# Kernel tuning notes

Hardware: AMD Instinct MI355X
Metric: run time of the kernel (lower is better)

Reference implementation:

```python
import jax, jax.numpy as jnp
import numpy as np

B, S, H, I, E = 4, 4096, 1024, 4096, 4
VOCAB = 32000


def setup_inputs() -> dict:
    key = jax.random.key(0)
    k1, k2, k3, k4, k5 = jax.random.split(key, 5)
    scale = 1.0 / np.sqrt(H)
    return {
        "hidden_states": jax.random.normal(k1, (B, S, H), dtype=jnp.float32),
        "gate_proj": jax.random.normal(k2, (E, H, I), dtype=jnp.float32) * scale,
        "up_proj": jax.random.normal(k3, (E, H, I), dtype=jnp.float32) * scale,
        "down_proj": jax.random.normal(k4, (E, I, H), dtype=jnp.float32) * (1.0 / np.sqrt(I)),
        "token_ids": jax.random.randint(k5, (B, S), 0, VOCAB, dtype=jnp.int64),
    }


def reference(hidden_states, gate_proj, up_proj, down_proj, token_ids):
    # hidden_states: [B, S, H]; token_ids: [B, S]
    num_experts = gate_proj.shape[0]
    expert_ids = token_ids % num_experts  # [B, S]
    out = jnp.zeros_like(hidden_states)
    for e in range(num_experts):  # small fixed expert loop
        gate = jax.nn.silu(jnp.einsum("bsh,hi->bsi", hidden_states, gate_proj[e]))
        up = jnp.einsum("bsh,hi->bsi", hidden_states, up_proj[e])
        y = jnp.einsum("bsi,ih->bsh", gate * up, down_proj[e])
        out = jnp.where((expert_ids == e)[..., None], y, out)
    return out
```

## Files before the change

kernel.cpp:

```cpp
#include <hip/hip_runtime.h>

#define TOK    16384
#define HD     1024
#define ID     4096
#define NE     4
#define MAXMT  131
#define MAXMT2 67
#define NKT    (HD / 64)

typedef __attribute__((ext_vector_type(4))) float f32x4;
typedef __attribute__((ext_vector_type(8))) short bf16x8;
typedef unsigned int u32;

static __device__ __forceinline__ unsigned short f2bf(float f) {
  unsigned u = __float_as_uint(f);
  u += 0x7FFFu + ((u >> 16) & 1u);
  return (unsigned short)(u >> 16);
}

static __device__ __forceinline__ void gl16(const void* g, void* l) {
  __builtin_amdgcn_global_load_lds((const __attribute__((address_space(1))) u32*)g,
                                   (__attribute__((address_space(3))) u32*)l, 16, 0, 0);
}

static __device__ __forceinline__ void barx() {
  asm volatile("" ::: "memory");
  __builtin_amdgcn_s_barrier();
  asm volatile("" ::: "memory");
}

__global__ void k_route0(const int* __restrict__ ids, int* __restrict__ meta) {
  __shared__ int cnt[4];
  int t = threadIdx.x;
  if (t < 4) cnt[t] = 0;
  __syncthreads();
  int l0 = 0, l1 = 0, l2 = 0, l3 = 0;
  for (int i = t; i < TOK; i += 256) {
    int e = ids[i] & 3;
    l0 += (e == 0); l1 += (e == 1); l2 += (e == 2); l3 += (e == 3);
  }
  atomicAdd(&cnt[0], l0); atomicAdd(&cnt[1], l1);
  atomicAdd(&cnt[2], l2); atomicAdd(&cnt[3], l3);
  __syncthreads();
  if (t == 0) {
    int o = 0;
    for (int e = 0; e < 4; ++e) { meta[e] = o; meta[8 + e] = o; o += cnt[e]; }
    meta[4] = o;
  }
}

__global__ void k_route1(const int* __restrict__ ids, int* __restrict__ meta,
                         int* __restrict__ perm) {
  int i = blockIdx.x * 256 + threadIdx.x;
  if (i < TOK) {
    int e = ids[i] & 3;
    int s = atomicAdd(&meta[8 + e], 1);
    perm[s] = i;
  }
}

__global__ void k_conv(const float* __restrict__ s, unsigned short* __restrict__ d, int n8) {
  int i = blockIdx.x * blockDim.x + threadIdx.x;
  int st = gridDim.x * blockDim.x;
  for (; i < n8; i += st) {
    const f32x4* p = (const f32x4*)(s + ((size_t)i << 3));
    f32x4 a = p[0], b = p[1];
    union { unsigned short u[8]; uint4 q; } o;
    o.u[0] = f2bf(a.x); o.u[1] = f2bf(a.y); o.u[2] = f2bf(a.z); o.u[3] = f2bf(a.w);
    o.u[4] = f2bf(b.x); o.u[5] = f2bf(b.y); o.u[6] = f2bf(b.z); o.u[7] = f2bf(b.w);
    *(uint4*)(d + ((size_t)i << 3)) = o.q;
  }
}

__global__ void k_tr12(const float* __restrict__ gw, const float* __restrict__ uw,
                       const float* __restrict__ dw, unsigned short* __restrict__ gT,
                       unsigned short* __restrict__ uT, unsigned short* __restrict__ dT) {
  __shared__ float tile[64][65];
  int z = blockIdx.y;
  const float* s; unsigned short* d; int R, C, lg;
  if (z < 8) {
    R = HD; C = ID; lg = 6;
    int m = z & 3;
    if (z < 4) { s = gw + (size_t)m * R * C; d = gT + (size_t)m * R * C; }
    else       { s = uw + (size_t)m * R * C; d = uT + (size_t)m * R * C; }
  } else {
    R = ID; C = HD; lg = 4;
    int m = z - 8;
    s = dw + (size_t)m * R * C; d = dT + (size_t)m * R * C;
  }
  int bx = blockIdx.x;
  int tx = bx & ((1 << lg) - 1), ty = bx >> lg;
  int r0 = ty << 6, c0 = tx << 6;
  int t = threadIdx.x;
  int lr = t >> 4, lc = (t & 15) << 2;
  #pragma unroll
  for (int it = 0; it < 4; ++it) {
    int r = lr + (it << 4);
    f32x4 v = *(const f32x4*)(s + (size_t)(r0 + r) * C + c0 + lc);
    tile[r][lc] = v.x; tile[r][lc + 1] = v.y; tile[r][lc + 2] = v.z; tile[r][lc + 3] = v.w;
  }
  __syncthreads();
  int c = t >> 2, rb = (t & 3) << 4;
  union { unsigned short u[16]; uint4 q[2]; } o;
  #pragma unroll
  for (int j = 0; j < 16; ++j) o.u[j] = f2bf(tile[rb + j][c]);
  uint4* dp = (uint4*)(d + (size_t)(c0 + c) * R + r0 + rb);
  dp[0] = o.q[0]; dp[1] = o.q[1];
}

#define MFMA16 __builtin_amdgcn_mfma_f32_16x16x32_bf16

#define RD_A(MH, KX, D) { _Pragma("unroll") for (int m = 0; m < 4; ++m) \
  fa[m] = *(const bf16x8*)(smem + (D) + ((offA[m] + (MH) * 8192) ^ ((KX) << 6))); }
#define RD_B(KX, D) { _Pragma("unroll") for (int n = 0; n < 4; ++n) \
  fb[n] = *(const bf16x8*)(smem + (D) + (offB[n] ^ ((KX) << 6))); }
#define STG_A(HH, TILE, D) { _Pragma("unroll") for (int j = (HH) * 2; j < (HH) * 2 + 2; ++j) \
  gl16(srcA[j] + (TILE) * 64, smem + (D) + dstA[j]); }
#define STG_B(HH, TILE, D) { _Pragma("unroll") for (int j = (HH) * 2; j < (HH) * 2 + 2; ++j) \
  gl16(srcB[j] + (TILE) * 64, smem + (D) + dstB[j]); }
#define PH_TAIL(MH) barx(); \
  asm volatile("s_waitcnt lgkmcnt(0)" ::: "memory"); \
  __builtin_amdgcn_sched_barrier(0); \
  __builtin_amdgcn_s_setprio(1); \
  { _Pragma("unroll") for (int m = 0; m < 4; ++m) \
    _Pragma("unroll") for (int n = 0; n < 4; ++n) \
      acc[(MH) * 4 + m][n] = MFMA16(fa[m], fb[n], acc[(MH) * 4 + m][n], 0, 0, 0); } \
  __builtin_amdgcn_s_setprio(0)

__global__ __launch_bounds__(512, 2) void k_gemm1(
    const unsigned short* __restrict__ hid,
    const unsigned short* __restrict__ gT,
    const unsigned short* __restrict__ uT,
    const int* __restrict__ meta,
    const int* __restrict__ perm,
    unsigned short* __restrict__ act) {
  extern __shared__ __align__(16) char smem[];
  int offs[5];
  #pragma unroll
  for (int i = 0; i < 5; ++i) offs[i] = meta[i];
  int bid = blockIdx.x;
  int logical = (bid & 7) * (MAXMT2 * 32 / 8) + (bid >> 3);
  int mt = logical >> 5;
  int ny = logical & 31;
  int e = -1, mloc = 0, base = 0;
  #pragma unroll
  for (int ee = 0; ee < 4; ++ee) {
    int tiles = (offs[ee + 1] - offs[ee] + 255) >> 8;
    if (e < 0 && mt < base + tiles) { e = ee; mloc = mt - base; }
    base += tiles;
  }
  if (e < 0) return;
  int slot0 = offs[e] + (mloc << 8);
  int send = offs[e + 1];
  int tid = threadIdx.x, lane = tid & 63, wid = tid >> 6;
  int n0 = ny << 7;

  int rsub = lane >> 3;
  int ke = ((lane & 7) ^ rsub) << 3;
  const unsigned short* srcA[4];
  const unsigned short* srcB[4];
  int dstA[4], dstB[4];
  const unsigned short* gb = gT + (size_t)e * ID * HD;
  const unsigned short* ub = uT + (size_t)e * ID * HD;
  #pragma unroll
  for (int j = 0; j < 4; ++j) {
    int r = j * 64 + wid * 8 + rsub;
    int slot = slot0 + r;
    int pr = perm[slot < send ? slot : slot0];
    srcA[j] = hid + (size_t)pr * HD + ke;
    dstA[j] = j * 8192 + wid * 1024;
    int rb = r;
    int s = rb >> 4;
    int grow = n0 + ((s >> 1) << 4) + (rb & 15);
    srcB[j] = ((s & 1) ? ub : gb) + (size_t)grow * HD + ke;
    dstB[j] = 32768 + j * 8192 + wid * 1024;
  }

  int wm = wid >> 2, wn = wid & 3;
  int r16 = lane & 15, kg = lane >> 4;
  int offA[4], offB[4];
  #pragma unroll
  for (int m = 0; m < 4; ++m) {
    int row = wm * 128 + m * 16 + r16;
    offA[m] = row * 128 + ((kg << 4) ^ ((row & 7) << 4));
  }
  #pragma unroll
  for (int n = 0; n < 4; ++n) {
    int row = wn * 64 + n * 16 + r16;
    offB[n] = 32768 + row * 128 + ((kg << 4) ^ ((row & 7) << 4));
  }

  f32x4 acc[8][4];
  #pragma unroll
  for (int m = 0; m < 8; ++m)
    #pragma unroll
    for (int n = 0; n < 4; ++n) acc[m][n] = (f32x4){0.f, 0.f, 0.f, 0.f};
  bf16x8 fa[4], fb[4];

  STG_B(0, 0, 0);
  STG_A(0, 0, 0); STG_A(1, 0, 0);
  STG_B(1, 0, 0);
  STG_B(0, 1, 65536);
  asm volatile("s_waitcnt vmcnt(2)" ::: "memory");
  barx();

  #pragma unroll 1
  for (int i = 0; i < NKT / 2 - 1; ++i) {
    int t1 = 2 * i + 1, t2 = 2 * i + 2, t3 = 2 * i + 3;
    RD_A(0, 0, 0); RD_B(0, 0);
    STG_B(1, t1, 65536);
    PH_TAIL(0); barx();
    RD_A(1, 0, 0);
    STG_A(0, t1, 65536); STG_A(1, t1, 65536);
    PH_TAIL(1); barx();
    RD_A(0, 1, 0); RD_B(1, 0);
    PH_TAIL(0); barx();
    RD_A(1, 1, 0);
    STG_B(0, t2, 0);
    PH_TAIL(1);
    asm volatile("s_waitcnt vmcnt(2)" ::: "memory");
    barx();
    RD_A(0, 0, 65536); RD_B(0, 65536);
    STG_A(0, t2, 0); STG_A(1, t2, 0);
    PH_TAIL(0); barx();
    RD_A(1, 0, 65536);
    STG_B(1, t2, 0);
    PH_TAIL(1); barx();
    RD_A(0, 1, 65536); RD_B(1, 65536);
    PH_TAIL(0); barx();
    RD_A(1, 1, 65536);
    STG_B(0, t3, 65536);
    PH_TAIL(1);
    asm volatile("s_waitcnt vmcnt(2)" ::: "memory");
    barx();
  }
  {
    RD_A(0, 0, 0); RD_B(0, 0);
    STG_B(1, 15, 65536);
    PH_TAIL(0); barx();
    RD_A(1, 0, 0);
    STG_A(0, 15, 65536); STG_A(1, 15, 65536);
    PH_TAIL(1); barx();
    RD_A(0, 1, 0); RD_B(1, 0);
    PH_TAIL(0); barx();
    RD_A(1, 1, 0);
    PH_TAIL(1);
    asm volatile("s_waitcnt vmcnt(0)" ::: "memory");
    barx();
    RD_A(0, 0, 65536); RD_B(0, 65536);
    PH_TAIL(0); barx();
    RD_A(1, 0, 65536);
    PH_TAIL(1); barx();
    RD_A(0, 1, 65536); RD_B(1, 65536);
    PH_TAIL(0); barx();
    RD_A(1, 1, 65536);
    PH_TAIL(1);
  }

  #pragma unroll
  for (int mf = 0; mf < 8; ++mf) {
    int lr = wm * 128 + mf * 16 + kg * 4;
    #pragma unroll
    for (int np = 0; np < 2; ++np) {
      int col = n0 + (2 * wn + np) * 16 + r16;
      #pragma unroll
      for (int r = 0; r < 4; ++r) {
        int slot = slot0 + lr + r;
        if (slot < send) {
          float g = acc[mf][2 * np][r];
          float u = acc[mf][2 * np + 1][r];
          float y = (g / (1.f + __expf(-g))) * u;
          act[(size_t)slot * ID + col] = f2bf(y);
        }
      }
    }
  }
}

__global__ __launch_bounds__(256, 2) void k_gemm2(
    const unsigned short* __restrict__ act,
    const unsigned short* __restrict__ dT,
    const int* __restrict__ meta,
    const int* __restrict__ perm,
    float* __restrict__ out) {
  __shared__ unsigned short As[128 * 64];
  __shared__ unsigned short Bs[128 * 64];
  int offs[5];
  #pragma unroll
  for (int i = 0; i < 5; ++i) offs[i] = meta[i];
  int bid = blockIdx.x;
  int logical = (bid & 7) * (MAXMT * 8 / 8) + (bid >> 3);
  int mt = logical >> 3;
  int nyy = logical & 7;
  int e = -1, mloc = 0, base = 0;
  #pragma unroll
  for (int ee = 0; ee < 4; ++ee) {
    int tiles = (offs[ee + 1] - offs[ee] + 127) >> 7;
    if (e < 0 && mt < base + tiles) { e = ee; mloc = mt - base; }
    base += tiles;
  }
  if (e < 0) return;
  int slot0 = offs[e] + (mloc << 7);
  int send = offs[e + 1];
  int tid = threadIdx.x;
  int n0 = nyy << 7;
  const unsigned short* dbase = dT + (size_t)e * HD * ID;
  const unsigned short* ap[4];
  const unsigned short* bp[4];
  int wofs[4];
  #pragma unroll
  for (int it = 0; it < 4; ++it) {
    int b = (tid << 4) + (it << 12);
    int row = b >> 7;
    int kob = b & 127;
    int slot = slot0 + row;
    int s2 = slot < send ? slot : slot0;
    ap[it] = act + (size_t)s2 * ID + (kob >> 1);
    bp[it] = dbase + (size_t)(n0 + row) * ID + (kob >> 1);
    wofs[it] = row * 64 + ((kob ^ ((row & 7) << 4)) >> 1);
  }
  int lane = tid & 63, wid = tid >> 6;
  int wm = wid >> 1, wn = wid & 1;
  int r16 = lane & 15, kg = lane >> 4;
  f32x4 zero = {0.f, 0.f, 0.f, 0.f};
  f32x4 acc[4][4];
  #pragma unroll
  for (int m = 0; m < 4; ++m)
    #pragma unroll
    for (int n = 0; n < 4; ++n) acc[m][n] = zero;

  bf16x8 sa[4], sb[4];
  #pragma unroll
  for (int it = 0; it < 4; ++it) {
    sa[it] = *(const bf16x8*)(ap[it]);
    sb[it] = *(const bf16x8*)(bp[it]);
  }
  for (int kt = 0; kt < ID / 64; ++kt) {
    __syncthreads();
    #pragma unroll
    for (int it = 0; it < 4; ++it) {
      *(bf16x8*)(As + wofs[it]) = sa[it];
      *(bf16x8*)(Bs + wofs[it]) = sb[it];
    }
    __syncthreads();
    if (kt < ID / 64 - 1) {
      int ko = (kt + 1) << 6;
      #pragma unroll
      for (int it = 0; it < 4; ++it) {
        sa[it] = *(const bf16x8*)(ap[it] + ko);
        sb[it] = *(const bf16x8*)(bp[it] + ko);
      }
    }
    #pragma unroll
    for (int kk = 0; kk < 2; ++kk) {
      bf16x8 fa[4], fb[4];
      #pragma unroll
      for (int m = 0; m < 4; ++m) {
        int row = (wm << 6) + (m << 4) + r16;
        int kob = (kk << 6) + (kg << 4);
        fa[m] = *(const bf16x8*)(As + row * 64 + ((kob ^ ((row & 7) << 4)) >> 1));
      }
      #pragma unroll
      for (int n = 0; n < 4; ++n) {
        int row = (wn << 6) + (n << 4) + r16;
        int kob = (kk << 6) + (kg << 4);
        fb[n] = *(const bf16x8*)(Bs + row * 64 + ((kob ^ ((row & 7) << 4)) >> 1));
      }
      #pragma unroll
      for (int m = 0; m < 4; ++m)
        #pragma unroll
        for (int n = 0; n < 4; ++n)
          acc[m][n] = __builtin_amdgcn_mfma_f32_16x16x32_bf16(fa[m], fb[n], acc[m][n], 0, 0, 0);
    }
  }
  #pragma unroll
  for (int m = 0; m < 4; ++m) {
    int lr = (wm << 6) + (m << 4) + (kg << 2);
    int pr4[4];
    #pragma unroll
    for (int r = 0; r < 4; ++r) {
      int slot = slot0 + lr + r;
      pr4[r] = slot < send ? perm[slot] : -1;
    }
    #pragma unroll
    for (int n = 0; n < 4; ++n) {
      int col = n0 + (wn << 6) + (n << 4) + r16;
      #pragma unroll
      for (int r = 0; r < 4; ++r) {
        if (pr4[r] >= 0) out[(size_t)pr4[r] * HD + col] = acc[m][n][r];
      }
    }
  }
}

extern "C" void kernel_launch(void* const* d_in, const int* in_sizes, int n_in,
                              void* d_out, int out_size, void* d_ws, size_t ws_size,
                              hipStream_t stream) {
  const float* hs = (const float*)d_in[0];
  const float* gw = (const float*)d_in[1];
  const float* uw = (const float*)d_in[2];
  const float* dw = (const float*)d_in[3];
  const int* ids = (const int*)d_in[4];
  float* out = (float*)d_out;

  char* w = (char*)d_ws;
  size_t o = 0;
  int* meta = (int*)(w + o); o += 64;
  int* perm = (int*)(w + o); o += (size_t)TOK * 4;
  o = (o + 255) & ~(size_t)255;
  unsigned short* hid = (unsigned short*)(w + o); o += (size_t)TOK * HD * 2;
  unsigned short* gT  = (unsigned short*)(w + o); o += (size_t)NE * ID * HD * 2;
  unsigned short* uT  = (unsigned short*)(w + o); o += (size_t)NE * ID * HD * 2;
  unsigned short* dT  = (unsigned short*)(w + o); o += (size_t)NE * ID * HD * 2;
  unsigned short* actb = (unsigned short*)(w + o); o += (size_t)TOK * ID * 2;

  hipFuncSetAttribute((const void*)k_gemm1,
                      hipFuncAttributeMaxDynamicSharedMemorySize, 131072);

  hipLaunchKernelGGL(k_route0, dim3(1), dim3(256), 0, stream, ids, meta);
  hipLaunchKernelGGL(k_route1, dim3(TOK / 256), dim3(256), 0, stream, ids, meta, perm);
  hipLaunchKernelGGL(k_conv, dim3(2048), dim3(256), 0, stream, hs, hid, TOK * HD / 8);
  hipLaunchKernelGGL(k_tr12, dim3(1024, 12), dim3(256), 0, stream, gw, uw, dw, gT, uT, dT);
  hipLaunchKernelGGL(k_gemm1, dim3(MAXMT2 * 32), dim3(512), 131072, stream,
                     hid, gT, uT, meta, perm, actb);
  hipLaunchKernelGGL(k_gemm2, dim3(MAXMT * 8), dim3(256), 0, stream,
                     actb, dT, meta, perm, out);
}
```

Baseline: 666.9 us.

## Restructure gemm1 pipeline to 4-stage K=32 ring buffer with double-buffered fragments

Replaces the two-stage K=64 LDS double buffer in the gate/up GEMM with a four-deep ring of K=32 tiles (32 KB each) and a new XOR swizzle sized for 64-byte rows. Register fragments are double-buffered (faX/faY, fbE/fbO), so LDS reads for the next MFMA cluster are issued before the current one and waited on with partial lgkmcnt counts. The aim is deeper global-load prefetch and better overlap of LDS reads with MFMA. In exchange it uses more fragment registers, issues more barriers per unit of K, and the clamped tail stages issue redundant loads.

```diff
diff --git a/kernel.cpp b/kernel.cpp
--- a/kernel.cpp
+++ b/kernel.cpp
@@ -6,7 +6,7 @@
 #define NE     4
 #define MAXMT  131
 #define MAXMT2 67
-#define NKT    (HD / 64)
+#define NT32   (HD / 32)
 
 typedef __attribute__((ext_vector_type(4))) float f32x4;
 typedef __attribute__((ext_vector_type(8))) short bf16x8;
@@ -109,22 +109,27 @@
 }
 
 #define MFMA16 __builtin_amdgcn_mfma_f32_16x16x32_bf16
-
-#define RD_A(MH, KX, D) { _Pragma("unroll") for (int m = 0; m < 4; ++m) \
-  fa[m] = *(const bf16x8*)(smem + (D) + ((offA[m] + (MH) * 8192) ^ ((KX) << 6))); }
-#define RD_B(KX, D) { _Pragma("unroll") for (int n = 0; n < 4; ++n) \
-  fb[n] = *(const bf16x8*)(smem + (D) + (offB[n] ^ ((KX) << 6))); }
-#define STG_A(HH, TILE, D) { _Pragma("unroll") for (int j = (HH) * 2; j < (HH) * 2 + 2; ++j) \
-  gl16(srcA[j] + (TILE) * 64, smem + (D) + dstA[j]); }
-#define STG_B(HH, TILE, D) { _Pragma("unroll") for (int j = (HH) * 2; j < (HH) * 2 + 2; ++j) \
-  gl16(srcB[j] + (TILE) * 64, smem + (D) + dstB[j]); }
-#define PH_TAIL(MH) barx(); \
-  asm volatile("s_waitcnt lgkmcnt(0)" ::: "memory"); \
+#define BASE4(T) (((T) & 3) * 32768)
+
+#define RD1(T, FA, FB) { const char* bb = smem + BASE4(T); \
+  _Pragma("unroll") for (int m = 0; m < 4; ++m) FA[m] = *(const bf16x8*)(bb + offA0[m]); \
+  _Pragma("unroll") for (int n = 0; n < 4; ++n) FB[n] = *(const bf16x8*)(bb + offB[n]); }
+
+#define RD2(T, FA) { const char* bb = smem + BASE4(T); \
+  _Pragma("unroll") for (int m = 0; m < 4; ++m) FA[m] = *(const bf16x8*)(bb + offA1[m]); }
+
+#define STG(T, H) { int tt = (T) < NT32 ? (T) : NT32 - 1; int ko = tt * 32; \
+  char* bb = smem + BASE4(T); \
+  gl16(srcA[H] + ko, bb + dA[H]); gl16(srcB[H] + ko, bb + dB[H]); }
+
+#define CLUSTER(FA, FB, MH, NW) \
+  barx(); \
+  asm volatile("s_waitcnt lgkmcnt(" #NW ")" ::: "memory"); \
   __builtin_amdgcn_sched_barrier(0); \
   __builtin_amdgcn_s_setprio(1); \
   { _Pragma("unroll") for (int m = 0; m < 4; ++m) \
     _Pragma("unroll") for (int n = 0; n < 4; ++n) \
-      acc[(MH) * 4 + m][n] = MFMA16(fa[m], fb[n], acc[(MH) * 4 + m][n], 0, 0, 0); } \
+      acc[(MH) * 4 + m][n] = MFMA16(FA[m], FB[n], acc[(MH) * 4 + m][n], 0, 0, 0); } \
   __builtin_amdgcn_s_setprio(0)
 
 __global__ __launch_bounds__(512, 2) void k_gemm1(
@@ -155,39 +160,40 @@
   int tid = threadIdx.x, lane = tid & 63, wid = tid >> 6;
   int n0 = ny << 7;
 
-  int rsub = lane >> 3;
-  int ke = ((lane & 7) ^ rsub) << 3;
-  const unsigned short* srcA[4];
-  const unsigned short* srcB[4];
-  int dstA[4], dstB[4];
+  int sslot = (tid & 3) ^ ((tid >> 3) & 3);
+  int ke = sslot << 3;
+  const unsigned short* srcA[2];
+  const unsigned short* srcB[2];
+  int dA[2], dB[2];
   const unsigned short* gb = gT + (size_t)e * ID * HD;
   const unsigned short* ub = uT + (size_t)e * ID * HD;
   #pragma unroll
-  for (int j = 0; j < 4; ++j) {
-    int r = j * 64 + wid * 8 + rsub;
+  for (int j = 0; j < 2; ++j) {
+    int r = (tid >> 2) + j * 128;
     int slot = slot0 + r;
     int pr = perm[slot < send ? slot : slot0];
     srcA[j] = hid + (size_t)pr * HD + ke;
-    dstA[j] = j * 8192 + wid * 1024;
-    int rb = r;
-    int s = rb >> 4;
-    int grow = n0 + ((s >> 1) << 4) + (rb & 15);
-    srcB[j] = ((s & 1) ? ub : gb) + (size_t)grow * HD + ke;
-    dstB[j] = 32768 + j * 8192 + wid * 1024;
+    dA[j] = (tid << 4) + j * 8192;
+    int sB = r >> 4;
+    int grow = n0 + ((sB >> 1) << 4) + (r & 15);
+    srcB[j] = ((sB & 1) ? ub : gb) + (size_t)grow * HD + ke;
+    dB[j] = 16384 + (tid << 4) + j * 8192;
   }
 
   int wm = wid >> 2, wn = wid & 3;
   int r16 = lane & 15, kg = lane >> 4;
-  int offA[4], offB[4];
+  int offA0[4], offA1[4], offB[4];
   #pragma unroll
   for (int m = 0; m < 4; ++m) {
-    int row = wm * 128 + m * 16 + r16;
-    offA[m] = row * 128 + ((kg << 4) ^ ((row & 7) << 4));
+    int r0 = wm * 128 + m * 16 + r16;
+    offA0[m] = r0 * 64 + ((kg << 4) ^ (((r0 >> 1) & 3) << 4));
+    int r1 = r0 + 64;
+    offA1[m] = r1 * 64 + ((kg << 4) ^ (((r1 >> 1) & 3) << 4));
   }
   #pragma unroll
   for (int n = 0; n < 4; ++n) {
-    int row = wn * 64 + n * 16 + r16;
-    offB[n] = 32768 + row * 128 + ((kg << 4) ^ ((row & 7) << 4));
+    int rb = wn * 64 + n * 16 + r16;
+    offB[n] = 16384 + rb * 64 + ((kg << 4) ^ (((rb >> 1) & 3) << 4));
   }
 
   f32x4 acc[8][4];
@@ -195,67 +201,34 @@
   for (int m = 0; m < 8; ++m)
     #pragma unroll
     for (int n = 0; n < 4; ++n) acc[m][n] = (f32x4){0.f, 0.f, 0.f, 0.f};
-  bf16x8 fa[4], fb[4];
-
-  STG_B(0, 0, 0);
-  STG_A(0, 0, 0); STG_A(1, 0, 0);
-  STG_B(1, 0, 0);
-  STG_B(0, 1, 65536);
-  asm volatile("s_waitcnt vmcnt(2)" ::: "memory");
+  bf16x8 faX[4], faY[4], fbE[4], fbO[4];
+
+  STG(0, 0); STG(0, 1);
+  STG(1, 0); STG(1, 1);
+  STG(2, 0);
+  asm volatile("s_waitcnt vmcnt(6)" ::: "memory");
   barx();
+  RD1(0, faX, fbE);
 
   #pragma unroll 1
-  for (int i = 0; i < NKT / 2 - 1; ++i) {
-    int t1 = 2 * i + 1, t2 = 2 * i + 2, t3 = 2 * i + 3;
-    RD_A(0, 0, 0); RD_B(0, 0);
-    STG_B(1, t1, 65536);
-    PH_TAIL(0); barx();
-    RD_A(1, 0, 0);
-    STG_A(0, t1, 65536); STG_A(1, t1, 65536);
-    PH_TAIL(1); barx();
-    RD_A(0, 1, 0); RD_B(1, 0);
-    PH_TAIL(0); barx();
-    RD_A(1, 1, 0);
-    STG_B(0, t2, 0);
-    PH_TAIL(1);
-    asm volatile("s_waitcnt vmcnt(2)" ::: "memory");
-    barx();
-    RD_A(0, 0, 65536); RD_B(0, 65536);
-    STG_A(0, t2, 0); STG_A(1, t2, 0);
-    PH_TAIL(0); barx();
-    RD_A(1, 0, 65536);
-    STG_B(1, t2, 0);
-    PH_TAIL(1); barx();
-    RD_A(0, 1, 65536); RD_B(1, 65536);
-    PH_TAIL(0); barx();
-    RD_A(1, 1, 65536);
-    STG_B(0, t3, 65536);
-    PH_TAIL(1);
-    asm volatile("s_waitcnt vmcnt(2)" ::: "memory");
-    barx();
-  }
-  {
-    RD_A(0, 0, 0); RD_B(0, 0);
-    STG_B(1, 15, 65536);
-    PH_TAIL(0); barx();
-    RD_A(1, 0, 0);
-    STG_A(0, 15, 65536); STG_A(1, 15, 65536);
-    PH_TAIL(1); barx();
-    RD_A(0, 1, 0); RD_B(1, 0);
-    PH_TAIL(0); barx();
-    RD_A(1, 1, 0);
-    PH_TAIL(1);
-    asm volatile("s_waitcnt vmcnt(0)" ::: "memory");
-    barx();
-    RD_A(0, 0, 65536); RD_B(0, 65536);
-    PH_TAIL(0); barx();
-    RD_A(1, 0, 65536);
-    PH_TAIL(1); barx();
-    RD_A(0, 1, 65536); RD_B(1, 65536);
-    PH_TAIL(0); barx();
-    RD_A(1, 1, 65536);
-    PH_TAIL(1);
-  }
+  for (int i = 0; i < NT32 / 2; ++i) {
+    int te = 2 * i, to = 2 * i + 1;
+    RD2(te, faY);
+    STG(te + 2, 1);
+    asm volatile("s_waitcnt vmcnt(4)" ::: "memory");
+    CLUSTER(faX, fbE, 0, 4);
+    RD1(to, faX, fbO);
+    STG(te + 3, 0);
+    CLUSTER(faY, fbE, 1, 8);
+    RD2(to, faY);
+    STG(te + 3, 1);
+    asm volatile("s_waitcnt vmcnt(4)" ::: "memory");
+    CLUSTER(faX, fbO, 0, 4);
+    RD1(te + 2, faX, fbE);
+    STG(te + 4, 0);
+    CLUSTER(faY, fbO, 1, 8);
+  }
+  asm volatile("s_waitcnt vmcnt(0) lgkmcnt(0)" ::: "memory");
 
   #pragma unroll
   for (int mf = 0; mf < 8; ++mf) {
```

New measurement: 694.0 us. 1.04x slower.

## Widen down-proj GEMM tile to 128x256 with 8 waves; fuse prep kernels

Applied to the files above, without the earlier changes.

The hidden-state bf16 conversion and the weight transpose kernels are merged into a single launch with a 2D grid, which removes one launch and lets the two overlap. The second GEMM now uses 512 threads, a 128x256 output tile and a larger B shared buffer. The grid drops to 524 blocks with a new XCD-aware mapping in which M tiles vary fastest, aiming for more reuse of A per loaded tile and better L2 locality. The cost is more LDS per block and fewer blocks in flight, which may reduce occupancy.

```diff
diff --git a/kernel.cpp b/kernel.cpp
--- a/kernel.cpp
+++ b/kernel.cpp
@@ -59,24 +59,23 @@
   }
 }
 
-__global__ void k_conv(const float* __restrict__ s, unsigned short* __restrict__ d, int n8) {
-  int i = blockIdx.x * blockDim.x + threadIdx.x;
-  int st = gridDim.x * blockDim.x;
-  for (; i < n8; i += st) {
-    const f32x4* p = (const f32x4*)(s + ((size_t)i << 3));
+__global__ void k_pre(const float* __restrict__ gw, const float* __restrict__ uw,
+                      const float* __restrict__ dw, const float* __restrict__ hs,
+                      unsigned short* __restrict__ gT, unsigned short* __restrict__ uT,
+                      unsigned short* __restrict__ dT, unsigned short* __restrict__ hid) {
+  int z = blockIdx.y;
+  int t = threadIdx.x;
+  if (z >= 12) {
+    int i = ((z - 12) * 1024 + blockIdx.x) * 256 + t;
+    const f32x4* p = (const f32x4*)(hs + ((size_t)i << 3));
     f32x4 a = p[0], b = p[1];
     union { unsigned short u[8]; uint4 q; } o;
     o.u[0] = f2bf(a.x); o.u[1] = f2bf(a.y); o.u[2] = f2bf(a.z); o.u[3] = f2bf(a.w);
     o.u[4] = f2bf(b.x); o.u[5] = f2bf(b.y); o.u[6] = f2bf(b.z); o.u[7] = f2bf(b.w);
-    *(uint4*)(d + ((size_t)i << 3)) = o.q;
-  }
-}
-
-__global__ void k_tr12(const float* __restrict__ gw, const float* __restrict__ uw,
-                       const float* __restrict__ dw, unsigned short* __restrict__ gT,
-                       unsigned short* __restrict__ uT, unsigned short* __restrict__ dT) {
+    *(uint4*)(hid + ((size_t)i << 3)) = o.q;
+    return;
+  }
   __shared__ float tile[64][65];
-  int z = blockIdx.y;
   const float* s; unsigned short* d; int R, C, lg;
   if (z < 8) {
     R = HD; C = ID; lg = 6;
@@ -91,7 +90,6 @@
   int bx = blockIdx.x;
   int tx = bx & ((1 << lg) - 1), ty = bx >> lg;
   int r0 = ty << 6, c0 = tx << 6;
-  int t = threadIdx.x;
   int lr = t >> 4, lc = (t & 15) << 2;
   #pragma unroll
   for (int it = 0; it < 4; ++it) {
@@ -277,21 +275,23 @@
   }
 }
 
-__global__ __launch_bounds__(256, 2) void k_gemm2(
+__global__ __launch_bounds__(512, 2) void k_gemm2(
     const unsigned short* __restrict__ act,
     const unsigned short* __restrict__ dT,
     const int* __restrict__ meta,
     const int* __restrict__ perm,
     float* __restrict__ out) {
   __shared__ unsigned short As[128 * 64];
-  __shared__ unsigned short Bs[128 * 64];
+  __shared__ unsigned short Bs[256 * 64];
   int offs[5];
   #pragma unroll
   for (int i = 0; i < 5; ++i) offs[i] = meta[i];
   int bid = blockIdx.x;
-  int logical = (bid & 7) * (MAXMT * 8 / 8) + (bid >> 3);
-  int mt = logical >> 3;
-  int nyy = logical & 7;
+  int xcd = bid & 7, off = bid >> 3;
+  int q = 524 / 8, r = 524 % 8;
+  int logical = (xcd < r ? xcd * (q + 1) : r * (q + 1) + (xcd - r) * q) + off;
+  int mt = logical % MAXMT;
+  int nyy = logical / MAXMT;
   int e = -1, mloc = 0, base = 0;
   #pragma unroll
   for (int ee = 0; ee < 4; ++ee) {
@@ -303,53 +303,56 @@
   int slot0 = offs[e] + (mloc << 7);
   int send = offs[e + 1];
   int tid = threadIdx.x;
-  int n0 = nyy << 7;
+  int n0 = nyy << 8;
   const unsigned short* dbase = dT + (size_t)e * HD * ID;
-  const unsigned short* ap[4];
+  const unsigned short* ap[2];
   const unsigned short* bp[4];
-  int wofs[4];
-  #pragma unroll
-  for (int it = 0; it < 4; ++it) {
-    int b = (tid << 4) + (it << 12);
+  int wofsA[2], wofsB[4];
+  #pragma unroll
+  for (int it = 0; it < 2; ++it) {
+    int b = (tid << 4) + (it << 13);
     int row = b >> 7;
     int kob = b & 127;
     int slot = slot0 + row;
     int s2 = slot < send ? slot : slot0;
     ap[it] = act + (size_t)s2 * ID + (kob >> 1);
+    wofsA[it] = row * 64 + ((kob ^ ((row & 7) << 4)) >> 1);
+  }
+  #pragma unroll
+  for (int it = 0; it < 4; ++it) {
+    int b = (tid << 4) + (it << 13);
+    int row = b >> 7;
+    int kob = b & 127;
     bp[it] = dbase + (size_t)(n0 + row) * ID + (kob >> 1);
-    wofs[it] = row * 64 + ((kob ^ ((row & 7) << 4)) >> 1);
+    wofsB[it] = row * 64 + ((kob ^ ((row & 7) << 4)) >> 1);
   }
   int lane = tid & 63, wid = tid >> 6;
-  int wm = wid >> 1, wn = wid & 1;
+  int wm = wid >> 2, wn = wid & 3;
   int r16 = lane & 15, kg = lane >> 4;
-  f32x4 zero = {0.f, 0.f, 0.f, 0.f};
   f32x4 acc[4][4];
   #pragma unroll
   for (int m = 0; m < 4; ++m)
     #pragma unroll
-    for (int n = 0; n < 4; ++n) acc[m][n] = zero;
-
-  bf16x8 sa[4], sb[4];
-  #pragma unroll
-  for (int it = 0; it < 4; ++it) {
-    sa[it] = *(const bf16x8*)(ap[it]);
-    sb[it] = *(const bf16x8*)(bp[it]);
-  }
+    for (int n = 0; n < 4; ++n) acc[m][n] = (f32x4){0.f, 0.f, 0.f, 0.f};
+
+  bf16x8 sa[2], sb[4];
+  #pragma unroll
+  for (int it = 0; it < 2; ++it) sa[it] = *(const bf16x8*)(ap[it]);
+  #pragma unroll
+  for (int it = 0; it < 4; ++it) sb[it] = *(const bf16x8*)(bp[it]);
   for (int kt = 0; kt < ID / 64; ++kt) {
     __syncthreads();
     #pragma unroll
-    for (int it = 0; it < 4; ++it) {
-      *(bf16x8*)(As + wofs[it]) = sa[it];
-      *(bf16x8*)(Bs + wofs[it]) = sb[it];
-    }
+    for (int it = 0; it < 2; ++it) *(bf16x8*)(As + wofsA[it]) = sa[it];
+    #pragma unroll
+    for (int it = 0; it < 4; ++it) *(bf16x8*)(Bs + wofsB[it]) = sb[it];
     __syncthreads();
     if (kt < ID / 64 - 1) {
       int ko = (kt + 1) << 6;
       #pragma unroll
-      for (int it = 0; it < 4; ++it) {
-        sa[it] = *(const bf16x8*)(ap[it] + ko);
-        sb[it] = *(const bf16x8*)(bp[it] + ko);
-      }
+      for (int it = 0; it < 2; ++it) sa[it] = *(const bf16x8*)(ap[it] + ko);
+      #pragma unroll
+      for (int it = 0; it < 4; ++it) sb[it] = *(const bf16x8*)(bp[it] + ko);
     }
     #pragma unroll
     for (int kk = 0; kk < 2; ++kk) {
@@ -370,7 +373,7 @@
       for (int m = 0; m < 4; ++m)
         #pragma unroll
         for (int n = 0; n < 4; ++n)
-          acc[m][n] = __builtin_amdgcn_mfma_f32_16x16x32_bf16(fa[m], fb[n], acc[m][n], 0, 0, 0);
+          acc[m][n] = MFMA16(fa[m], fb[n], acc[m][n], 0, 0, 0);
     }
   }
   #pragma unroll
@@ -378,16 +381,16 @@
     int lr = (wm << 6) + (m << 4) + (kg << 2);
     int pr4[4];
     #pragma unroll
-    for (int r = 0; r < 4; ++r) {
-      int slot = slot0 + lr + r;
-      pr4[r] = slot < send ? perm[slot] : -1;
+    for (int rr = 0; rr < 4; ++rr) {
+      int slot = slot0 + lr + rr;
+      pr4[rr] = slot < send ? perm[slot] : -1;
     }
     #pragma unroll
     for (int n = 0; n < 4; ++n) {
       int col = n0 + (wn << 6) + (n << 4) + r16;
       #pragma unroll
-      for (int r = 0; r < 4; ++r) {
-        if (pr4[r] >= 0) out[(size_t)pr4[r] * HD + col] = acc[m][n][r];
+      for (int rr = 0; rr < 4; ++rr) {
+        if (pr4[rr] >= 0) out[(size_t)pr4[rr] * HD + col] = acc[m][n][rr];
       }
     }
   }
@@ -419,10 +422,10 @@
 
   hipLaunchKernelGGL(k_route0, dim3(1), dim3(256), 0, stream, ids, meta);
   hipLaunchKernelGGL(k_route1, dim3(TOK / 256), dim3(256), 0, stream, ids, meta, perm);
-  hipLaunchKernelGGL(k_conv, dim3(2048), dim3(256), 0, stream, hs, hid, TOK * HD / 8);
-  hipLaunchKernelGGL(k_tr12, dim3(1024, 12), dim3(256), 0, stream, gw, uw, dw, gT, uT, dT);
+  hipLaunchKernelGGL(k_pre, dim3(1024, 20), dim3(256), 0, stream,
+                     gw, uw, dw, hs, gT, uT, dT, hid);
   hipLaunchKernelGGL(k_gemm1, dim3(MAXMT2 * 32), dim3(512), 131072, stream,
                      hid, gT, uT, meta, perm, actb);
-  hipLaunchKernelGGL(k_gemm2, dim3(MAXMT * 8), dim3(256), 0, stream,
+  hipLaunchKernelGGL(k_gemm2, dim3(524), dim3(512), 0, stream,
                      actb, dT, meta, perm, out);
 }
```

Result: slower. 771.1 us (+15.6%).
